# Kernel tuning notes

Hardware: AMD Instinct MI355X
Metric: run time of the kernel (lower is better)

## Reference

```python
import jax, jax.numpy as jnp
import numpy as np

NUM_LABELS_I = 28  # 7 entity types * 4 (B/I/E/S)
NUM_LABELS = 31    # + O, EOS, BOS
INDEX_O, INDEX_EOS, INDEX_BOS = 28, 29, 30
NEG = -10000.0


def _make_trans(rng):
    # replicate ChainCRF4NestedNER.reset_parameters() structural masking
    bs = np.arange(0, NUM_LABELS_I, 4)
    is_ = bs + 1
    es = bs + 2
    ss = bs + 3
    t = (rng.standard_normal((NUM_LABELS, NUM_LABELS)) * 0.1).astype(np.float32)
    for i in bs:
        t[i, :i + 1] = NEG; t[i, i + 3:] = NEG
    for i in is_:
        t[i, :i] = NEG; t[i, i + 2:] = NEG
    for i in np.concatenate([es, ss, [INDEX_O]]):
        t[i, is_] = NEG; t[i, es] = NEG; t[i, INDEX_BOS] = NEG
    t[INDEX_EOS, :INDEX_EOS] = NEG; t[INDEX_EOS, INDEX_BOS] = NEG
    t[INDEX_BOS, is_] = NEG; t[INDEX_BOS, es] = NEG; t[INDEX_BOS, INDEX_BOS] = NEG
    return jnp.asarray(t)


def setup_inputs() -> dict:
    B, T, D = 64, 512, 768
    key = jax.random.key(0)
    k1, k2, k3 = jax.random.split(key, 3)
    inp = jax.random.normal(k1, (B, T, D), dtype=jnp.float32)
    target = jax.random.randint(k2, (B, T), 0, 29, dtype=jnp.int64)  # real labels + O only
    mask = jnp.ones((B, T), dtype=jnp.float32)
    state_w = jax.random.normal(k3, (NUM_LABELS, D), dtype=jnp.float32) * 0.02
    state_b = jnp.concatenate([jnp.zeros(INDEX_EOS, jnp.float32),
                               jnp.full(NUM_LABELS - INDEX_EOS, NEG, jnp.float32)])
    trans = _make_trans(np.random.default_rng(0))
    return {"input": inp, "target": target, "mask": mask,
            "state_w": state_w, "state_b": state_b, "trans": trans}


def reference(input, target, mask, state_w, state_b, trans):
    B, T, _ = input.shape
    # state scores [B, T, L]
    out_s = jnp.einsum('btd,ld->btl', input, state_w) + state_b
    out_s = out_s.at[:, :, INDEX_EOS].add((mask == 0).astype(out_s.dtype) * 20000.0)
    # energy [B, T, L, L]: trans[prev, curr] + state[curr]
    energy = trans[None, None, :, :] + out_s[:, :, None, :]
    # forward algorithm (logsumexp semiring) as a scan over time
    energy_t = jnp.moveaxis(energy, 1, 0)  # [T, B, L, L]
    part0 = energy_t[0, :, INDEX_BOS, :]   # [B, L]

    def step(part, e_t):
        new = jax.nn.logsumexp(e_t + part[:, :, None], axis=1)
        return new, None

    partition, _ = jax.lax.scan(step, part0, energy_t[1:])
    # gold-path energy: sum_t energy[b, t, prev_label, label]
    prev = jnp.concatenate([jnp.full((B, 1), INDEX_BOS, dtype=target.dtype),
                            target[:, :-1]], axis=1)
    bi = jnp.arange(B)[:, None]
    ti = jnp.arange(T)[None, :]
    tgt_energy = energy[bi, ti, prev, target].sum(axis=1)
    loss = jax.nn.logsumexp(trans[:, INDEX_EOS][None, :] + partition, axis=1) - tgt_energy
    return loss, energy
```

## Files before the change

### kernel.cpp

```cpp
#include <hip/hip_runtime.h>

typedef float f32x4  __attribute__((ext_vector_type(4)));
typedef float f32x16 __attribute__((ext_vector_type(16)));
typedef short s16x8  __attribute__((ext_vector_type(8)));

constexpr int NL  = 31;
constexpr int BB  = 64;
constexpr int TT  = 512;
constexpr int DD  = 768;
constexpr int RTOT = BB * TT;
constexpr int IDX_EOS = 29;
constexpr int IDX_BOS = 30;
constexpr float LOG2E = 1.4426950408889634f;
constexpr float LN2F  = 0.6931471805599453f;

union Frag8 { unsigned u[4]; s16x8 s; };

__device__ inline unsigned pk2(float a, float b) {
  unsigned ua = __float_as_uint(a), ub = __float_as_uint(b);
  ua = (ua + 0x7fffu + ((ua >> 16) & 1u)) >> 16;
  ub = (ub + 0x7fffu + ((ub >> 16) & 1u)) >> 16;
  return ua | (ub << 16);
}
__device__ inline unsigned short bf16r(float a) {
  unsigned ua = __float_as_uint(a);
  return (unsigned short)((ua + 0x7fffu + ((ua >> 16) & 1u)) >> 16);
}

__device__ inline float bfly_max32(float v) {
#define STEPM(K) { float o = __int_as_float(__builtin_amdgcn_ds_swizzle(__float_as_int(v), ((K) << 10) | 0x1f)); v = fmaxf(v, o); }
  STEPM(1) STEPM(2) STEPM(4) STEPM(8) STEPM(16)
#undef STEPM
  return v;
}
__device__ inline float bfly_sum32(float v) {
#define STEPS(K) { float o = __int_as_float(__builtin_amdgcn_ds_swizzle(__float_as_int(v), ((K) << 10) | 0x1f)); v = v + o; }
  STEPS(1) STEPS(2) STEPS(4) STEPS(8) STEPS(16)
#undef STEPS
  return v;
}

__device__ inline void repack(const float E[16], int h, Frag8& B1, Frag8& B2) {
  unsigned o1a = pk2(E[4 * h], E[4 * h + 1]), o1b = pk2(E[4 * h + 2], E[4 * h + 3]);
  unsigned o2a = pk2(E[8 + 4 * h], E[8 + 4 * h + 1]), o2b = pk2(E[8 + 4 * h + 2], E[8 + 4 * h + 3]);
  int hb = 4 * (1 - h);
  unsigned s1a = pk2(E[hb], E[hb + 1]),         s1b = pk2(E[hb + 2], E[hb + 3]);
  unsigned s2a = pk2(E[8 + hb], E[8 + hb + 1]), s2b = pk2(E[8 + hb + 2], E[8 + hb + 3]);
  unsigned r1a = __shfl_xor((int)s1a, 32), r1b = __shfl_xor((int)s1b, 32);
  unsigned r2a = __shfl_xor((int)s2a, 32), r2b = __shfl_xor((int)s2b, 32);
  if (h == 0) {
    B1.u[0] = o1a; B1.u[1] = o1b; B1.u[2] = r1a; B1.u[3] = r1b;
    B2.u[0] = o2a; B2.u[1] = o2b; B2.u[2] = r2a; B2.u[3] = r2b;
  } else {
    B1.u[0] = r1a; B1.u[1] = r1b; B1.u[2] = o1a; B1.u[3] = o1b;
    B2.u[0] = r2a; B2.u[1] = r2b; B2.u[2] = o2a; B2.u[3] = o2b;
  }
}

__device__ inline void renorm16(float E[16], float& Sacc) {
  float m = E[0];
#pragma unroll
  for (int r = 1; r < 16; ++r) m = fmaxf(m, E[r]);
  m = bfly_max32(m);
  m = fmaxf(m, __shfl_xor(m, 32));
  float lg = truncf(log2f(m));
  Sacc += lg;
  float sc = exp2f(-lg);
#pragma unroll
  for (int r = 0; r < 16; ++r) E[r] *= sc;
}

__device__ inline void load_A16(const unsigned short* M, int l, int h, Frag8& A1, Frag8& A2) {
  A1.s = *(const s16x8*)(M + l * 32 + 8 * h);
  A2.s = *(const s16x8*)(M + l * 32 + 16 + 8 * h);
}
__device__ inline void load_B16(const unsigned short* M, int l, int h, Frag8& B1, Frag8& B2) {
#pragma unroll
  for (int m = 0; m < 4; ++m) {
    int k = 8 * h + 2 * m;
    unsigned lo0 = M[k * 32 + l],        hi0 = M[(k + 1) * 32 + l];
    unsigned lo1 = M[(k + 16) * 32 + l], hi1 = M[(k + 17) * 32 + l];
    B1.u[m] = lo0 | (hi0 << 16);
    B2.u[m] = lo1 | (hi1 << 16);
  }
}

__global__ void k_prep(const float* __restrict__ sw, unsigned short* __restrict__ Bw) {
  for (int i = blockIdx.x * 256 + threadIdx.x; i < 32 * DD; i += 8 * 256)
    Bw[i] = (i < NL * DD) ? bf16r(sw[i]) : (unsigned short)0;
}

__global__ __launch_bounds__(256) void k_outs(
    const float* __restrict__ inp, const unsigned short* __restrict__ Bw,
    const float* __restrict__ sb, const float* __restrict__ msk,
    const float* __restrict__ trans, const int* __restrict__ target,
    float* __restrict__ outs, float* __restrict__ energy,
    float* __restrict__ ws_partial)
{
  __shared__ __align__(16) unsigned short As[16 * 72];
  __shared__ float tr[961];
  __shared__ float osh[16 * NL];
  int tid = threadIdx.x, wave = tid >> 6, lane = tid & 63;
  int r0 = blockIdx.x * 16;

  if (wave) {
    for (int idx = tid - 64; idx < 961; idx += 192) tr[idx] = trans[idx];
  } else {
    int quad = lane >> 4, l15 = lane & 15;
    int srow = lane >> 2, scol = lane & 3;
    const float* gsrc = inp + (size_t)(r0 + srow) * DD + scol * 4;
    unsigned* dw = (unsigned*)As;
    int wbase = srow * 36 + scol * 2;

    f32x4 pre[4];
#pragma unroll
    for (int i = 0; i < 4; ++i) pre[i] = *(const f32x4*)(gsrc + i * 16);

    f32x4 acc[2] = {};
    for (int kc = 0; kc < 12; ++kc) {
#pragma unroll
      for (int i = 0; i < 4; ++i) {
        dw[wbase + i * 8]     = pk2(pre[i][0], pre[i][1]);
        dw[wbase + i * 8 + 1] = pk2(pre[i][2], pre[i][3]);
      }
      if (kc < 11) {
        const float* g2 = gsrc + (kc + 1) * 64;
#pragma unroll
        for (int i = 0; i < 4; ++i) pre[i] = *(const f32x4*)(g2 + i * 16);
      }
#pragma unroll
      for (int ks = 0; ks < 2; ++ks) {
        s16x8 af = *(const s16x8*)((const unsigned short*)As + l15 * 72 + ks * 32 + quad * 8);
#pragma unroll
        for (int ct = 0; ct < 2; ++ct) {
          s16x8 bf = *(const s16x8*)(Bw + (ct * 16 + l15) * DD + kc * 64 + ks * 32 + quad * 8);
          acc[ct] = __builtin_amdgcn_mfma_f32_16x16x32_bf16(af, bf, acc[ct], 0, 0, 0);
        }
      }
    }
#pragma unroll
    for (int ct = 0; ct < 2; ++ct) {
      int n = ct * 16 + l15;
      if (n < NL) {
        float b = sb[n];
#pragma unroll
        for (int r = 0; r < 4; ++r) {
          int lr = quad * 4 + r;
          int row = r0 + lr;
          float v = acc[ct][r] + b;
          if (n == IDX_EOS && msk[row] == 0.f) v += 20000.f;
          osh[lr * NL + n] = v;
          outs[(size_t)row * NL + n] = v;
        }
      }
    }
  }
  __syncthreads();

  if (tid < 16) {
    int r = r0 + tid;
    int tg = target[r];
    int prv = ((r & (TT - 1)) == 0) ? IDX_BOS : target[r - 1];
    float cc = tr[prv * NL + tg] + osh[tid * NL + tg];
#pragma unroll
    for (int off = 8; off; off >>= 1) cc += __shfl_down(cc, off);
    if (tid == 0) ws_partial[blockIdx.x] = cc;
  }

  float* dst = energy + (size_t)r0 * 961;
#pragma unroll 5
  for (int it = 0; it < 15; ++it) {
    int v = it * 256 + tid;
    int e = v * 4;
    f32x4 val;
#pragma unroll
    for (int k = 0; k < 4; ++k) {
      unsigned x = e + k;
      unsigned q = __umulhi(x, 4469269u);
      unsigned c = x - q * 961u;
      unsigned j = c - 31u * ((c * 67651u) >> 21);
      val[k] = tr[c] + osh[q * NL + j];
    }
    *(f32x4*)(dst + e) = val;
  }
  if (tid < 4) {
    int e = (3840 + tid) * 4;
    f32x4 val;
#pragma unroll
    for (int k = 0; k < 4; ++k) {
      unsigned x = e + k;
      unsigned q = __umulhi(x, 4469269u);
      unsigned c = x - q * 961u;
      unsigned j = c - 31u * ((c * 67651u) >> 21);
      val[k] = tr[c] + osh[q * NL + j];
    }
    *(f32x4*)(dst + e) = val;
  }
}

__global__ __launch_bounds__(256) void k_seg(
    const float* __restrict__ outs, const float* __restrict__ trans,
    unsigned short* __restrict__ Mq16, float* __restrict__ Sq)
{
  __shared__ float ub4[4][256];
  __shared__ __align__(16) unsigned short Ms[4][1024];
  __shared__ float Ss[4];
  int tid = threadIdx.x, wave = tid >> 6, lane = tid & 63;
  int l = lane & 31, h = lane >> 5;
  int unit = blockIdx.x * 4 + wave;
  int b = unit >> 6, c = unit & 63;
  int t0 = 1 + c * 8;
  int n = (c == 63) ? 7 : 8;

  float* ub = ub4[wave];
#pragma unroll
  for (int it = 0; it < 4; ++it) {
    int idx = lane + it * 64;
    int row = idx >> 5, col = idx & 31;
    float v = 0.f;
    if (col < NL && row < n)
      v = exp2f(LOG2E * outs[((size_t)b * TT + t0 + row) * NL + col]);
    ub[idx] = v;
  }

  Frag8 A1, A2, B1, B2;
#pragma unroll
  for (int m = 0; m < 4; ++m) {
    int k0 = 8 * h + 2 * m, k1 = k0 + 1;
    float a0 = (k0 < NL && l < NL) ? exp2f(LOG2E * trans[k0 * NL + l]) : 0.f;
    float a1 = (k1 < NL && l < NL) ? exp2f(LOG2E * trans[k1 * NL + l]) : 0.f;
    A1.u[m] = pk2(a0, a1);
    int k2 = 16 + k0, k3 = 16 + k1;
    float a2 = (k2 < NL && l < NL) ? exp2f(LOG2E * trans[k2 * NL + l]) : 0.f;
    float a3 = (k3 < NL && l < NL) ? exp2f(LOG2E * trans[k3 * NL + l]) : 0.f;
    A2.u[m] = pk2(a2, a3);
    B1.u[m] = ((k0 == l) ? 0x3f80u : 0u) | (((k1 == l) ? 0x3f80u : 0u) << 16);
    B2.u[m] = ((k2 == l) ? 0x3f80u : 0u) | (((k3 == l) ? 0x3f80u : 0u) << 16);
  }

  float E[16];
  for (int s = 0; s < n; ++s) {
    const float* us = ub + s * 32 + 4 * h;
    f32x4 u0 = *(const f32x4*)(us);
    f32x4 u1 = *(const f32x4*)(us + 8);
    f32x4 u2 = *(const f32x4*)(us + 16);
    f32x4 u3 = *(const f32x4*)(us + 24);
    f32x16 D = {};
    D = __builtin_amdgcn_mfma_f32_32x32x16_bf16(A1.s, B1.s, D, 0, 0, 0);
    D = __builtin_amdgcn_mfma_f32_32x32x16_bf16(A2.s, B2.s, D, 0, 0, 0);
#pragma unroll
    for (int jj = 0; jj < 4; ++jj) {
      E[jj]      = D[jj]      * u0[jj];
      E[4 + jj]  = D[4 + jj]  * u1[jj];
      E[8 + jj]  = D[8 + jj]  * u2[jj];
      E[12 + jj] = D[12 + jj] * u3[jj];
    }
    if (s + 1 < n) repack(E, h, B1, B2);
  }
  float S = 0.f;
  renorm16(E, S);
  unsigned short* mo = Ms[wave];
#pragma unroll
  for (int r = 0; r < 16; ++r) {
    int row = (r & 3) + 8 * (r >> 2) + 4 * h;
    mo[row * 32 + l] = bf16r(E[r]);
  }
  if (lane == 0) Ss[wave] = S;
  __syncthreads();

  if (wave == 0) {
    load_B16(Ms[0], l, h, B1, B2);
    float Sx = Ss[0] + Ss[1] + Ss[2] + Ss[3];
    float E2[16];
#pragma unroll
    for (int i = 1; i < 4; ++i) {
      load_A16(Ms[i], l, h, A1, A2);
      f32x16 D = {};
      D = __builtin_amdgcn_mfma_f32_32x32x16_bf16(A1.s, B1.s, D, 0, 0, 0);
      D = __builtin_amdgcn_mfma_f32_32x32x16_bf16(A2.s, B2.s, D, 0, 0, 0);
#pragma unroll
      for (int r = 0; r < 16; ++r) E2[r] = D[r];
      if (i < 3) repack(E2, h, B1, B2);
    }
    renorm16(E2, Sx);
    unsigned short* qo = Mq16 + (size_t)blockIdx.x * 1024;
#pragma unroll
    for (int r = 0; r < 16; ++r) {
      int row = (r & 3) + 8 * (r >> 2) + 4 * h;
      qo[row * 32 + l] = bf16r(E2[r]);
    }
    if (lane == 0) Sq[blockIdx.x] = Sx;
  }
}

__global__ __launch_bounds__(256) void k_tree2(
    const float* __restrict__ outs, const float* __restrict__ trans,
    const unsigned short* __restrict__ Mq16, const float* __restrict__ Sq,
    const float* __restrict__ ws_partial, float* __restrict__ loss)
{
  int tid = threadIdx.x, wave = tid >> 6, lane = tid & 63;
  int l = lane & 31, h = lane >> 5;
  int b = blockIdx.x * 4 + wave;
  const unsigned short* base = Mq16 + (size_t)b * 16384;
  Frag8 A1, A2, B1, B2;
  load_B16(base, l, h, B1, B2);
  float S = 0.f;
#pragma unroll
  for (int q = 0; q < 16; ++q) S += Sq[b * 16 + q];
  float E[16];
  for (int i = 1; i < 16; ++i) {
    load_A16(base + i * 1024, l, h, A1, A2);
    f32x16 D = {};
    D = __builtin_amdgcn_mfma_f32_32x32x16_bf16(A1.s, B1.s, D, 0, 0, 0);
    D = __builtin_amdgcn_mfma_f32_32x32x16_bf16(A2.s, B2.s, D, 0, 0, 0);
#pragma unroll
    for (int r = 0; r < 16; ++r) E[r] = D[r];
    if ((i & 3) == 3) renorm16(E, S);
    if (i < 15) repack(E, h, B1, B2);
  }
  float p0 = (l < NL) ? exp2f(LOG2E * (trans[IDX_BOS * NL + l] + outs[(size_t)b * TT * NL + l])) : 0.f;
  float sum_h = 0.f;
#pragma unroll
  for (int r = 0; r < 16; ++r) {
    float s = bfly_sum32(E[r] * p0);
    int row = (r & 3) + 8 * (r >> 2) + 4 * h;
    float We = (row < NL) ? exp2f(LOG2E * trans[row * NL + IDX_EOS]) : 0.f;
    sum_h += s * We;
  }
  float tot = sum_h + __shfl_xor(sum_h, 32);
  if (lane == 0) {
    float wst = 0.f;
#pragma unroll
    for (int i = 0; i < 32; ++i) wst += ws_partial[b * 32 + i];
    loss[b] = LN2F * (S + log2f(tot)) - wst;
  }
}

extern "C" void kernel_launch(void* const* d_in, const int* in_sizes, int n_in,
                              void* d_out, int out_size, void* d_ws, size_t ws_size,
                              hipStream_t stream) {
  const float* inp   = (const float*)d_in[0];
  const int*   tgt   = (const int*)d_in[1];
  const float* msk   = (const float*)d_in[2];
  const float* sw    = (const float*)d_in[3];
  const float* sb    = (const float*)d_in[4];
  const float* trans = (const float*)d_in[5];

  float* out    = (float*)d_out;
  float* loss   = out;
  float* energy = out + BB;

  float* outs        = (float*)d_ws;
  float* Sq          = outs + (size_t)RTOT * NL;
  float* ws_partial  = Sq + 1024;
  unsigned short* Mq16 = (unsigned short*)(ws_partial + 2048);
  unsigned short* Bw   = Mq16 + (size_t)1024 * 1024;

  k_prep<<<8, 256, 0, stream>>>(sw, Bw);
  k_outs<<<RTOT / 16, 256, 0, stream>>>(inp, Bw, sb, msk, trans, tgt, outs, energy, ws_partial);
  k_seg<<<1024, 256, 0, stream>>>(outs, trans, Mq16, Sq);
  k_tree2<<<16, 256, 0, stream>>>(outs, trans, Mq16, Sq, ws_partial, loss);
}
```

Before: 311.5 us.

## Fuse segment matrix products into GEMM kernel and use parallel tree reduction

Result: faster. 264.2 us (-15.2%).

```diff
diff --git a/kernel.cpp b/kernel.cpp
--- a/kernel.cpp
+++ b/kernel.cpp
@@ -85,57 +85,77 @@
   }
 }
 
+__device__ inline void tree_node(unsigned short* Tb, float* Ts, int ja, int jb, int l, int h) {
+  Frag8 A1, A2, B1, B2;
+  load_A16(Tb + ja * 1024, l, h, A1, A2);
+  load_B16(Tb + jb * 1024, l, h, B1, B2);
+  f32x16 D = {};
+  D = __builtin_amdgcn_mfma_f32_32x32x16_bf16(A1.s, B1.s, D, 0, 0, 0);
+  D = __builtin_amdgcn_mfma_f32_32x32x16_bf16(A2.s, B2.s, D, 0, 0, 0);
+  float E[16];
+#pragma unroll
+  for (int r = 0; r < 16; ++r) E[r] = D[r];
+  float S = Ts[ja] + Ts[jb];
+  renorm16(E, S);
+#pragma unroll
+  for (int r = 0; r < 16; ++r) {
+    int row = (r & 3) + 8 * (r >> 2) + 4 * h;
+    Tb[jb * 1024 + row * 32 + l] = bf16r(E[r]);
+  }
+  if (l == 0 && h == 0) Ts[jb] = S;
+}
+
 __global__ void k_prep(const float* __restrict__ sw, unsigned short* __restrict__ Bw) {
   for (int i = blockIdx.x * 256 + threadIdx.x; i < 32 * DD; i += 8 * 256)
     Bw[i] = (i < NL * DD) ? bf16r(sw[i]) : (unsigned short)0;
 }
 
-__global__ __launch_bounds__(256) void k_outs(
+__global__ __launch_bounds__(256) void k_fused(
     const float* __restrict__ inp, const unsigned short* __restrict__ Bw,
     const float* __restrict__ sb, const float* __restrict__ msk,
     const float* __restrict__ trans, const int* __restrict__ target,
-    float* __restrict__ outs, float* __restrict__ energy,
-    float* __restrict__ ws_partial)
+    float* __restrict__ energy, float* __restrict__ ws_partial,
+    unsigned short* __restrict__ Mb, float* __restrict__ Sb,
+    float* __restrict__ out0)
 {
-  __shared__ __align__(16) unsigned short As[16 * 72];
   __shared__ float tr[961];
   __shared__ float osh[16 * NL];
+  __shared__ float ubw[4][128];
+  __shared__ __align__(16) unsigned short Ms[4][1024];
+  __shared__ float Ss[4];
   int tid = threadIdx.x, wave = tid >> 6, lane = tid & 63;
-  int r0 = blockIdx.x * 16;
+  int bid = blockIdx.x;
+  int r0 = bid * 16;
 
   if (wave) {
     for (int idx = tid - 64; idx < 961; idx += 192) tr[idx] = trans[idx];
   } else {
     int quad = lane >> 4, l15 = lane & 15;
-    int srow = lane >> 2, scol = lane & 3;
-    const float* gsrc = inp + (size_t)(r0 + srow) * DD + scol * 4;
-    unsigned* dw = (unsigned*)As;
-    int wbase = srow * 36 + scol * 2;
-
-    f32x4 pre[4];
-#pragma unroll
-    for (int i = 0; i < 4; ++i) pre[i] = *(const f32x4*)(gsrc + i * 16);
+    const float* arow = inp + (size_t)(r0 + l15) * DD + quad * 8;
+
+    f32x4 pa0a = *(const f32x4*)(arow);
+    f32x4 pa0b = *(const f32x4*)(arow + 4);
+    f32x4 pa1a = *(const f32x4*)(arow + 32);
+    f32x4 pa1b = *(const f32x4*)(arow + 36);
 
     f32x4 acc[2] = {};
     for (int kc = 0; kc < 12; ++kc) {
-#pragma unroll
-      for (int i = 0; i < 4; ++i) {
-        dw[wbase + i * 8]     = pk2(pre[i][0], pre[i][1]);
-        dw[wbase + i * 8 + 1] = pk2(pre[i][2], pre[i][3]);
+      Frag8 af0, af1;
+      af0.u[0] = pk2(pa0a[0], pa0a[1]); af0.u[1] = pk2(pa0a[2], pa0a[3]);
+      af0.u[2] = pk2(pa0b[0], pa0b[1]); af0.u[3] = pk2(pa0b[2], pa0b[3]);
+      af1.u[0] = pk2(pa1a[0], pa1a[1]); af1.u[1] = pk2(pa1a[2], pa1a[3]);
+      af1.u[2] = pk2(pa1b[0], pa1b[1]); af1.u[3] = pk2(pa1b[2], pa1b[3]);
+      if (kc < 11) {
+        const float* a2 = arow + (kc + 1) * 64;
+        pa0a = *(const f32x4*)(a2);      pa0b = *(const f32x4*)(a2 + 4);
+        pa1a = *(const f32x4*)(a2 + 32); pa1b = *(const f32x4*)(a2 + 36);
       }
-      if (kc < 11) {
-        const float* g2 = gsrc + (kc + 1) * 64;
-#pragma unroll
-        for (int i = 0; i < 4; ++i) pre[i] = *(const f32x4*)(g2 + i * 16);
-      }
-#pragma unroll
-      for (int ks = 0; ks < 2; ++ks) {
-        s16x8 af = *(const s16x8*)((const unsigned short*)As + l15 * 72 + ks * 32 + quad * 8);
-#pragma unroll
-        for (int ct = 0; ct < 2; ++ct) {
-          s16x8 bf = *(const s16x8*)(Bw + (ct * 16 + l15) * DD + kc * 64 + ks * 32 + quad * 8);
-          acc[ct] = __builtin_amdgcn_mfma_f32_16x16x32_bf16(af, bf, acc[ct], 0, 0, 0);
-        }
+#pragma unroll
+      for (int ct = 0; ct < 2; ++ct) {
+        s16x8 bf0 = *(const s16x8*)(Bw + (ct * 16 + l15) * DD + kc * 64 + quad * 8);
+        acc[ct] = __builtin_amdgcn_mfma_f32_16x16x32_bf16(af0.s, bf0, acc[ct], 0, 0, 0);
+        s16x8 bf1 = *(const s16x8*)(Bw + (ct * 16 + l15) * DD + kc * 64 + 32 + quad * 8);
+        acc[ct] = __builtin_amdgcn_mfma_f32_16x16x32_bf16(af1.s, bf1, acc[ct], 0, 0, 0);
       }
     }
 #pragma unroll
@@ -146,16 +166,16 @@
 #pragma unroll
         for (int r = 0; r < 4; ++r) {
           int lr = quad * 4 + r;
-          int row = r0 + lr;
           float v = acc[ct][r] + b;
-          if (n == IDX_EOS && msk[row] == 0.f) v += 20000.f;
+          if (n == IDX_EOS && msk[r0 + lr] == 0.f) v += 20000.f;
           osh[lr * NL + n] = v;
-          outs[(size_t)row * NL + n] = v;
         }
       }
     }
   }
   __syncthreads();
+
+  if ((bid & 31) == 0 && tid < NL) out0[(bid >> 5) * NL + tid] = osh[tid];
 
   if (tid < 16) {
     int r = r0 + tid;
@@ -164,7 +184,7 @@
     float cc = tr[prv * NL + tg] + osh[tid * NL + tg];
 #pragma unroll
     for (int off = 8; off; off >>= 1) cc += __shfl_down(cc, off);
-    if (tid == 0) ws_partial[blockIdx.x] = cc;
+    if (tid == 0) ws_partial[bid] = cc;
   }
 
   float* dst = energy + (size_t)r0 * 961;
@@ -196,79 +216,70 @@
     }
     *(f32x4*)(dst + e) = val;
   }
-}
-
-__global__ __launch_bounds__(256) void k_seg(
-    const float* __restrict__ outs, const float* __restrict__ trans,
-    unsigned short* __restrict__ Mq16, float* __restrict__ Sq)
-{
-  __shared__ float ub4[4][256];
-  __shared__ __align__(16) unsigned short Ms[4][1024];
-  __shared__ float Ss[4];
-  int tid = threadIdx.x, wave = tid >> 6, lane = tid & 63;
-  int l = lane & 31, h = lane >> 5;
-  int unit = blockIdx.x * 4 + wave;
-  int b = unit >> 6, c = unit & 63;
-  int t0 = 1 + c * 8;
-  int n = (c == 63) ? 7 : 8;
-
-  float* ub = ub4[wave];
-#pragma unroll
-  for (int it = 0; it < 4; ++it) {
-    int idx = lane + it * 64;
-    int row = idx >> 5, col = idx & 31;
-    float v = 0.f;
-    if (col < NL && row < n)
-      v = exp2f(LOG2E * outs[((size_t)b * TT + t0 + row) * NL + col]);
-    ub[idx] = v;
-  }
-
-  Frag8 A1, A2, B1, B2;
-#pragma unroll
-  for (int m = 0; m < 4; ++m) {
-    int k0 = 8 * h + 2 * m, k1 = k0 + 1;
-    float a0 = (k0 < NL && l < NL) ? exp2f(LOG2E * trans[k0 * NL + l]) : 0.f;
-    float a1 = (k1 < NL && l < NL) ? exp2f(LOG2E * trans[k1 * NL + l]) : 0.f;
-    A1.u[m] = pk2(a0, a1);
-    int k2 = 16 + k0, k3 = 16 + k1;
-    float a2 = (k2 < NL && l < NL) ? exp2f(LOG2E * trans[k2 * NL + l]) : 0.f;
-    float a3 = (k3 < NL && l < NL) ? exp2f(LOG2E * trans[k3 * NL + l]) : 0.f;
-    A2.u[m] = pk2(a2, a3);
-    B1.u[m] = ((k0 == l) ? 0x3f80u : 0u) | (((k1 == l) ? 0x3f80u : 0u) << 16);
-    B2.u[m] = ((k2 == l) ? 0x3f80u : 0u) | (((k3 == l) ? 0x3f80u : 0u) << 16);
-  }
-
-  float E[16];
-  for (int s = 0; s < n; ++s) {
-    const float* us = ub + s * 32 + 4 * h;
-    f32x4 u0 = *(const f32x4*)(us);
-    f32x4 u1 = *(const f32x4*)(us + 8);
-    f32x4 u2 = *(const f32x4*)(us + 16);
-    f32x4 u3 = *(const f32x4*)(us + 24);
-    f32x16 D = {};
-    D = __builtin_amdgcn_mfma_f32_32x32x16_bf16(A1.s, B1.s, D, 0, 0, 0);
-    D = __builtin_amdgcn_mfma_f32_32x32x16_bf16(A2.s, B2.s, D, 0, 0, 0);
-#pragma unroll
-    for (int jj = 0; jj < 4; ++jj) {
-      E[jj]      = D[jj]      * u0[jj];
-      E[4 + jj]  = D[4 + jj]  * u1[jj];
-      E[8 + jj]  = D[8 + jj]  * u2[jj];
-      E[12 + jj] = D[12 + jj] * u3[jj];
-    }
-    if (s + 1 < n) repack(E, h, B1, B2);
-  }
-  float S = 0.f;
-  renorm16(E, S);
-  unsigned short* mo = Ms[wave];
-#pragma unroll
-  for (int r = 0; r < 16; ++r) {
-    int row = (r & 3) + 8 * (r >> 2) + 4 * h;
-    mo[row * 32 + l] = bf16r(E[r]);
-  }
-  if (lane == 0) Ss[wave] = S;
+
+  {
+    int l = lane & 31, h = lane >> 5;
+    int s0 = (bid % 32 == 0 && wave == 0) ? 1 : 0;
+
+    float* ub = ubw[wave];
+#pragma unroll
+    for (int it = 0; it < 2; ++it) {
+      int idx = lane + it * 64;
+      int row = idx >> 5, col = idx & 31;
+      float v = 0.f;
+      if (col < NL) v = exp2f(LOG2E * osh[(4 * wave + row) * NL + col]);
+      ub[idx] = v;
+    }
+
+    Frag8 A1, A2, B1, B2;
+#pragma unroll
+    for (int m = 0; m < 4; ++m) {
+      int k0 = 8 * h + 2 * m, k1 = k0 + 1;
+      float a0 = (k0 < NL && l < NL) ? exp2f(LOG2E * tr[k0 * NL + l]) : 0.f;
+      float a1 = (k1 < NL && l < NL) ? exp2f(LOG2E * tr[k1 * NL + l]) : 0.f;
+      A1.u[m] = pk2(a0, a1);
+      int k2 = 16 + k0, k3 = 16 + k1;
+      float a2 = (k2 < NL && l < NL) ? exp2f(LOG2E * tr[k2 * NL + l]) : 0.f;
+      float a3 = (k3 < NL && l < NL) ? exp2f(LOG2E * tr[k3 * NL + l]) : 0.f;
+      A2.u[m] = pk2(a2, a3);
+      B1.u[m] = ((k0 == l) ? 0x3f80u : 0u) | (((k1 == l) ? 0x3f80u : 0u) << 16);
+      B2.u[m] = ((k2 == l) ? 0x3f80u : 0u) | (((k3 == l) ? 0x3f80u : 0u) << 16);
+    }
+
+    float E[16];
+    for (int s = s0; s < 4; ++s) {
+      const float* us = ub + s * 32 + 4 * h;
+      f32x4 u0 = *(const f32x4*)(us);
+      f32x4 u1 = *(const f32x4*)(us + 8);
+      f32x4 u2 = *(const f32x4*)(us + 16);
+      f32x4 u3 = *(const f32x4*)(us + 24);
+      f32x16 D = {};
+      D = __builtin_amdgcn_mfma_f32_32x32x16_bf16(A1.s, B1.s, D, 0, 0, 0);
+      D = __builtin_amdgcn_mfma_f32_32x32x16_bf16(A2.s, B2.s, D, 0, 0, 0);
+#pragma unroll
+      for (int jj = 0; jj < 4; ++jj) {
+        E[jj]      = D[jj]      * u0[jj];
+        E[4 + jj]  = D[4 + jj]  * u1[jj];
+        E[8 + jj]  = D[8 + jj]  * u2[jj];
+        E[12 + jj] = D[12 + jj] * u3[jj];
+      }
+      if (s < 3) repack(E, h, B1, B2);
+    }
+    float S = 0.f;
+    renorm16(E, S);
+    unsigned short* mo = Ms[wave];
+#pragma unroll
+    for (int r = 0; r < 16; ++r) {
+      int row = (r & 3) + 8 * (r >> 2) + 4 * h;
+      mo[row * 32 + l] = bf16r(E[r]);
+    }
+    if (lane == 0) Ss[wave] = S;
+  }
   __syncthreads();
 
   if (wave == 0) {
+    int l = lane & 31, h = lane >> 5;
+    Frag8 A1, A2, B1, B2;
     load_B16(Ms[0], l, h, B1, B2);
     float Sx = Ss[0] + Ss[1] + Ss[2] + Ss[3];
     float E2[16];
@@ -283,56 +294,78 @@
       if (i < 3) repack(E2, h, B1, B2);
     }
     renorm16(E2, Sx);
-    unsigned short* qo = Mq16 + (size_t)blockIdx.x * 1024;
+    unsigned short* qo = Mb + (size_t)bid * 1024;
 #pragma unroll
     for (int r = 0; r < 16; ++r) {
       int row = (r & 3) + 8 * (r >> 2) + 4 * h;
       qo[row * 32 + l] = bf16r(E2[r]);
     }
-    if (lane == 0) Sq[blockIdx.x] = Sx;
-  }
-}
-
-__global__ __launch_bounds__(256) void k_tree2(
-    const float* __restrict__ outs, const float* __restrict__ trans,
-    const unsigned short* __restrict__ Mq16, const float* __restrict__ Sq,
-    const float* __restrict__ ws_partial, float* __restrict__ loss)
+    if (lane == 0) Sb[bid] = Sx;
+  }
+}
+
+__global__ __launch_bounds__(256) void k_tree(
+    const float* __restrict__ trans, const unsigned short* __restrict__ Mb,
+    const float* __restrict__ Sb, const float* __restrict__ ws_partial,
+    const float* __restrict__ out0, float* __restrict__ loss)
 {
+  __shared__ __align__(16) unsigned short T[32][1024];
+  __shared__ float Ts[32];
+  __shared__ float wsh[32];
   int tid = threadIdx.x, wave = tid >> 6, lane = tid & 63;
   int l = lane & 31, h = lane >> 5;
-  int b = blockIdx.x * 4 + wave;
-  const unsigned short* base = Mq16 + (size_t)b * 16384;
-  Frag8 A1, A2, B1, B2;
-  load_B16(base, l, h, B1, B2);
-  float S = 0.f;
-#pragma unroll
-  for (int q = 0; q < 16; ++q) S += Sq[b * 16 + q];
-  float E[16];
-  for (int i = 1; i < 16; ++i) {
-    load_A16(base + i * 1024, l, h, A1, A2);
+  int b = blockIdx.x;
+
+  const f32x4* src = (const f32x4*)(Mb + (size_t)b * 32 * 1024);
+  f32x4* dstT = (f32x4*)T;
+#pragma unroll
+  for (int i = 0; i < 16; ++i) dstT[tid + i * 256] = src[tid + i * 256];
+  if (tid < 32) {
+    Ts[tid] = Sb[b * 32 + tid];
+    wsh[tid] = ws_partial[b * 32 + tid];
+  }
+  __syncthreads();
+
+  unsigned short* T0 = T[0];
+#pragma unroll
+  for (int i = 0; i < 4; ++i) { int j = wave + 4 * i; tree_node(T0, Ts, 2 * j + 1, 2 * j, l, h); }
+  __syncthreads();
+#pragma unroll
+  for (int i = 0; i < 2; ++i) { int j = wave + 4 * i; tree_node(T0, Ts, 4 * j + 2, 4 * j, l, h); }
+  __syncthreads();
+  { int j = wave; tree_node(T0, Ts, 8 * j + 4, 8 * j, l, h); }
+  __syncthreads();
+  if (wave < 2) { int j = wave; tree_node(T0, Ts, 16 * j + 8, 16 * j, l, h); }
+  __syncthreads();
+
+  if (wave == 0) {
+    Frag8 A1, A2, B1, B2;
+    load_A16(T0 + 16 * 1024, l, h, A1, A2);
+    load_B16(T0, l, h, B1, B2);
     f32x16 D = {};
     D = __builtin_amdgcn_mfma_f32_32x32x16_bf16(A1.s, B1.s, D, 0, 0, 0);
     D = __builtin_amdgcn_mfma_f32_32x32x16_bf16(A2.s, B2.s, D, 0, 0, 0);
+    float E[16];
 #pragma unroll
     for (int r = 0; r < 16; ++r) E[r] = D[r];
-    if ((i & 3) == 3) renorm16(E, S);
-    if (i < 15) repack(E, h, B1, B2);
-  }
-  float p0 = (l < NL) ? exp2f(LOG2E * (trans[IDX_BOS * NL + l] + outs[(size_t)b * TT * NL + l])) : 0.f;
-  float sum_h = 0.f;
-#pragma unroll
-  for (int r = 0; r < 16; ++r) {
-    float s = bfly_sum32(E[r] * p0);
-    int row = (r & 3) + 8 * (r >> 2) + 4 * h;
-    float We = (row < NL) ? exp2f(LOG2E * trans[row * NL + IDX_EOS]) : 0.f;
-    sum_h += s * We;
-  }
-  float tot = sum_h + __shfl_xor(sum_h, 32);
-  if (lane == 0) {
-    float wst = 0.f;
-#pragma unroll
-    for (int i = 0; i < 32; ++i) wst += ws_partial[b * 32 + i];
-    loss[b] = LN2F * (S + log2f(tot)) - wst;
+    float S = Ts[0] + Ts[16];
+
+    float p0 = (l < NL) ? exp2f(LOG2E * (trans[IDX_BOS * NL + l] + out0[b * NL + l])) : 0.f;
+    float sum_h = 0.f;
+#pragma unroll
+    for (int r = 0; r < 16; ++r) {
+      float s = bfly_sum32(E[r] * p0);
+      int row = (r & 3) + 8 * (r >> 2) + 4 * h;
+      float We = (row < NL) ? exp2f(LOG2E * trans[row * NL + IDX_EOS]) : 0.f;
+      sum_h += s * We;
+    }
+    float tot = sum_h + __shfl_xor(sum_h, 32);
+    if (lane == 0) {
+      float wst = 0.f;
+#pragma unroll
+      for (int i = 0; i < 32; ++i) wst += wsh[i];
+      loss[b] = LN2F * (S + log2f(tot)) - wst;
+    }
   }
 }
 
@@ -350,14 +383,14 @@
   float* loss   = out;
   float* energy = out + BB;
 
-  float* outs        = (float*)d_ws;
-  float* Sq          = outs + (size_t)RTOT * NL;
-  float* ws_partial  = Sq + 1024;
-  unsigned short* Mq16 = (unsigned short*)(ws_partial + 2048);
-  unsigned short* Bw   = Mq16 + (size_t)1024 * 1024;
+  float* ws_partial = (float*)d_ws;
+  float* Sb   = ws_partial + 2048;
+  float* out0 = Sb + 2048;
+  unsigned short* Mb = (unsigned short*)(out0 + 2048);
+  unsigned short* Bw = Mb + (size_t)2048 * 1024;
 
   k_prep<<<8, 256, 0, stream>>>(sw, Bw);
-  k_outs<<<RTOT / 16, 256, 0, stream>>>(inp, Bw, sb, msk, trans, tgt, outs, energy, ws_partial);
-  k_seg<<<1024, 256, 0, stream>>>(outs, trans, Mq16, Sq);
-  k_tree2<<<16, 256, 0, stream>>>(outs, trans, Mq16, Sq, ws_partial, loss);
-}
+  k_fused<<<RTOT / 16, 256, 0, stream>>>(inp, Bw, sb, msk, trans, tgt,
+                                         energy, ws_partial, Mb, Sb, out0);
+  k_tree<<<BB, 256, 0, stream>>>(trans, Mb, Sb, ws_partial, out0, loss);
+}
```
